# Kernel tuning notes

Hardware: AMD Instinct MI355X
Metric: run time of the kernel (lower is better)

The kernel has to match this reference:

```python
import jax, jax.numpy as jnp
import numpy as np

NNZ = 3355443          # int(4096*4096*(1-0.8))
IN_FEATURES = 4096
OUT_FEATURES = 4096
BATCH = 64
ACTIVE_THRESHOLD = 0.01


def setup_inputs() -> dict:
    key = jax.random.key(0)
    k1, k2, k3, k4 = jax.random.split(key, 4)
    x = jax.random.uniform(k1, (BATCH, IN_FEATURES), dtype=jnp.float32)
    row_indices = jax.random.randint(k2, (NNZ,), 0, OUT_FEATURES, dtype=jnp.int32)
    col_indices = jax.random.randint(k3, (NNZ,), 0, IN_FEATURES, dtype=jnp.int32)
    values = jax.random.normal(k4, (NNZ,), dtype=jnp.float32)
    bias = jnp.zeros((OUT_FEATURES,), dtype=jnp.float32)
    return {"x": x, "row_indices": row_indices, "col_indices": col_indices,
            "values": values, "bias": bias}


def reference(x, row_indices, col_indices, values, bias):
    # Event-driven gating: only columns with x > threshold contribute.
    # Equivalent to masking x, then a standard COO spmv per batch row.
    xm = jnp.where(x > ACTIVE_THRESHOLD, x, jnp.zeros((), x.dtype))   # [B, in]
    contrib = values[None, :] * xm[:, col_indices]                    # [B, nnz]
    out = jnp.zeros((x.shape[0], bias.shape[0]), dtype=x.dtype)
    out = out.at[:, row_indices].add(contrib)                         # scatter-add over rows
    return out + bias[None, :]
```

## Files before the change

### kernel.cpp

```cpp
#include <hip/hip_runtime.h>
#include <hip/hip_bf16.h>
#include <stdint.h>

#define IN_F 4096
#define OUT_F 4096
#define NBKT 256
#define SBLOCKS 410
#define REC_PER_SB 8192
#define SMAX 14336u
#define THRESH 0.01f

typedef unsigned int u32;
typedef unsigned short u16;
typedef unsigned char u8;
typedef __attribute__((ext_vector_type(8))) short short8;
typedef __attribute__((ext_vector_type(4))) float f32x4;

static constexpr size_t pad256(size_t x) { return (x + 255u) & ~(size_t)255u; }
static constexpr size_t WS_XB   = 0;
static constexpr size_t WS_CUR  = pad256(WS_XB + (size_t)512 * 64 * 8 * 2);
static constexpr size_t WS_BINS = pad256(WS_CUR + (size_t)NBKT * 4);
static constexpr size_t WS_NEEDED = WS_BINS + (size_t)NBKT * SMAX * 4;

static __device__ __forceinline__ u16 f2bf(float v) {
  __hip_bfloat16 h = __float2bfloat16(v);
  return *reinterpret_cast<u16*>(&h);
}

__global__ __launch_bounds__(256) void k_init(u32* __restrict__ gcursor) {
  gcursor[threadIdx.x] = 0u;
}

__global__ __launch_bounds__(1024) void k_scatter(const int* __restrict__ rows,
                                                  const int* __restrict__ cols,
                                                  const float* __restrict__ vals, u32 nnz,
                                                  const float* __restrict__ x,
                                                  u16* __restrict__ xB,
                                                  u32* __restrict__ gcursor,
                                                  u32* __restrict__ sortb) {
  __shared__ u32 cnt[NBKT];
  __shared__ u32 pref[NBKT + 1];
  __shared__ u32 gbase[NBKT];
  __shared__ u32 srt[REC_PER_SB];
  __shared__ u8 srtb[REC_PER_SB];
  const int tid = threadIdx.x;
  const int lane = tid & 63;
  const int wid = tid >> 6;

  if (blockIdx.x < 32) {
    const int g = blockIdx.x * 1024 + tid;
    const int b = g & 63;
    const int kg = g >> 6;
    const float* src = x + (size_t)b * IN_F + kg * 8;
    const f32x4 a0 = *reinterpret_cast<const f32x4*>(src);
    const f32x4 a1 = *reinterpret_cast<const f32x4*>(src + 4);
    short8 o;
#pragma unroll
    for (int e = 0; e < 4; ++e) {
      float v = a0[e]; v = (v > THRESH) ? v : 0.0f; o[e] = (short)f2bf(v);
    }
#pragma unroll
    for (int e = 0; e < 4; ++e) {
      float v = a1[e]; v = (v > THRESH) ? v : 0.0f; o[4 + e] = (short)f2bf(v);
    }
    *reinterpret_cast<short8*>(xB + ((size_t)kg * 64 + b) * 8) = o;
  }

  if (tid < NBKT) cnt[tid] = 0;
  __syncthreads();
  const u32 base_i = blockIdx.x * (u32)REC_PER_SB;
  u32 rec[8], bkt[8], rk[8];
#pragma unroll
  for (int j = 0; j < 8; ++j) {
    const u32 i = base_i + (u32)j * 1024u + tid;
    bkt[j] = 0xffffffffu;
    if (i < nnz) {
      const u32 r = (u32)rows[i] & 4095u;
      const u32 c = (u32)cols[i] & 4095u;
      rec[j] = (c << 20) | ((r & 15u) << 16) | (u32)f2bf(vals[i]);
      bkt[j] = r >> 4;
      rk[j] = atomicAdd(&cnt[bkt[j]], 1u);
    }
  }
  __syncthreads();
  if (wid == 0) {
    u32 a[4]; u32 s = 0;
#pragma unroll
    for (int j = 0; j < 4; ++j) { a[j] = cnt[lane * 4 + j]; s += a[j]; }
    u32 xx = s;
#pragma unroll
    for (int d = 1; d < 64; d <<= 1) {
      const u32 y = (u32)__shfl_up((int)xx, d, 64);
      if (lane >= d) xx += y;
    }
    u32 e = xx - s;
#pragma unroll
    for (int j = 0; j < 4; ++j) { pref[lane * 4 + j] = e; e += a[j]; }
    if (lane == 63) pref[256] = e;
  }
  __syncthreads();
#pragma unroll
  for (int j = 0; j < 8; ++j)
    if (bkt[j] != 0xffffffffu) {
      const u32 pos = pref[bkt[j]] + rk[j];
      srt[pos] = rec[j];
      srtb[pos] = (u8)bkt[j];
    }
  if (tid < NBKT) {
    const u32 len = pref[tid + 1] - pref[tid];
    gbase[tid] = len ? atomicAdd(&gcursor[tid], len) : 0u;
  }
  __syncthreads();
  const u32 tot = pref[NBKT];
#pragma unroll
  for (int j = 0; j < 8; ++j) {
    const u32 i = (u32)j * 1024u + tid;
    if (i < tot) {
      const u32 t = srtb[i];
      const u32 off = gbase[t] + (i - pref[t]);
      if (off < SMAX) sortb[(size_t)t * SMAX + off] = srt[i];
    }
  }
}

__global__ __launch_bounds__(1024, 1) void k_accum(const u32* __restrict__ sortb,
                                                   const u32* __restrict__ ntot,
                                                   const u16* __restrict__ xB,
                                                   const float* __restrict__ bias,
                                                   float* __restrict__ out) {
  __shared__ float W[16 * 1024];
  const int tid = threadIdx.x;
  const int lane = tid & 63;
  const int w = tid >> 6;
  const u32 t = blockIdx.x;
  u32 n = ntot[t];
  if (n > SMAX) n = SMAX;
  const u32* bin = sortb + (size_t)t * SMAX;
  u32 rec[14];
#pragma unroll
  for (int j = 0; j < 14; ++j) {
    const u32 i = (u32)j * 1024u + tid;
    rec[j] = (i < n) ? bin[i] : 0u;
  }

  f32x4 acc0 = {0.f, 0.f, 0.f, 0.f}, acc1 = {0.f, 0.f, 0.f, 0.f};
  f32x4 acc2 = {0.f, 0.f, 0.f, 0.f}, acc3 = {0.f, 0.f, 0.f, 0.f};
  const int row = lane & 15;
  const int e8 = (lane >> 4) * 8;

  for (int q = 0; q < 4; ++q) {
    __syncthreads();
    const f32x4 z = {0.f, 0.f, 0.f, 0.f};
#pragma unroll
    for (int j = 0; j < 4; ++j)
      *reinterpret_cast<f32x4*>(&W[j * 4096 + tid * 4]) = z;
    __syncthreads();
#pragma unroll
    for (int j = 0; j < 14; ++j) {
      const u32 i = (u32)j * 1024u + tid;
      if (i < n) {
        const u32 rc = rec[j];
        if ((rc >> 30) == (u32)q) {
          const u32 rl = (rc >> 16) & 15u;
          const u32 cl = ((rc >> 20) & 1023u) ^ ((rl & 7u) << 3);
          __hip_atomic_fetch_add(&W[rl * 1024u + cl], __uint_as_float(rc << 16),
                                 __ATOMIC_RELAXED, __HIP_MEMORY_SCOPE_WORKGROUP);
        }
      }
    }
    __syncthreads();
#pragma unroll
    for (int s = 0; s < 2; ++s) {
      const int klb = w * 64 + s * 32 + e8;
      const int sw = klb ^ ((row & 7) << 3);
      const f32x4 wa = *reinterpret_cast<const f32x4*>(&W[row * 1024 + sw]);
      const f32x4 wb = *reinterpret_cast<const f32x4*>(&W[row * 1024 + (sw + 4)]);
      short8 af;
#pragma unroll
      for (int e = 0; e < 4; ++e) af[e] = (short)f2bf(wa[e]);
#pragma unroll
      for (int e = 0; e < 4; ++e) af[4 + e] = (short)f2bf(wb[e]);
      const int kabs = q * 1024 + klb;
      const u16* bp = xB + (size_t)(kabs >> 3) * 512 + (u32)row * 8;
      const short8 b0 = *reinterpret_cast<const short8*>(bp);
      const short8 b1 = *reinterpret_cast<const short8*>(bp + 128);
      const short8 b2 = *reinterpret_cast<const short8*>(bp + 256);
      const short8 b3 = *reinterpret_cast<const short8*>(bp + 384);
      acc0 = __builtin_amdgcn_mfma_f32_16x16x32_bf16(af, b0, acc0, 0, 0, 0);
      acc1 = __builtin_amdgcn_mfma_f32_16x16x32_bf16(af, b1, acc1, 0, 0, 0);
      acc2 = __builtin_amdgcn_mfma_f32_16x16x32_bf16(af, b2, acc2, 0, 0, 0);
      acc3 = __builtin_amdgcn_mfma_f32_16x16x32_bf16(af, b3, acc3, 0, 0, 0);
    }
  }
  __syncthreads();
  {
    const int ccol = lane & 15;
    const int rb = (lane >> 4) * 4;
#pragma unroll
    for (int qq = 0; qq < 4; ++qq) W[((w * 4 + 0) * 16 + rb + qq) * 16 + ccol] = acc0[qq];
#pragma unroll
    for (int qq = 0; qq < 4; ++qq) W[((w * 4 + 1) * 16 + rb + qq) * 16 + ccol] = acc1[qq];
#pragma unroll
    for (int qq = 0; qq < 4; ++qq) W[((w * 4 + 2) * 16 + rb + qq) * 16 + ccol] = acc2[qq];
#pragma unroll
    for (int qq = 0; qq < 4; ++qq) W[((w * 4 + 3) * 16 + rb + qq) * 16 + ccol] = acc3[qq];
  }
  __syncthreads();
  const int rl = tid & 15;
  const int b = tid >> 4;
  float sum = bias[t * 16u + rl];
#pragma unroll
  for (int w2 = 0; w2 < 16; ++w2)
    sum += W[((w2 * 4 + (b >> 4)) * 16 + rl) * 16 + (b & 15)];
  out[(size_t)b * OUT_F + t * 16u + rl] = sum;
}

__global__ __launch_bounds__(256) void k_bias_init(const float* __restrict__ bias,
                                                   float* __restrict__ out) {
  const int i = blockIdx.x * 256 + threadIdx.x;
  if (i < 64 * OUT_F) out[i] = bias[i & (OUT_F - 1)];
}

__global__ __launch_bounds__(256) void k_fallback(const int* __restrict__ rows,
                                                  const int* __restrict__ cols,
                                                  const float* __restrict__ vals,
                                                  const float* __restrict__ x,
                                                  float* __restrict__ out, int nnz) {
  const int gw = (int)(((u32)blockIdx.x * blockDim.x + threadIdx.x) >> 6);
  const int lane = threadIdx.x & 63;
  const int nw = (int)(((u32)gridDim.x * blockDim.x) >> 6);
  for (int i = gw; i < nnz; i += nw) {
    const int r = rows[i];
    const int c = cols[i];
    const float v = vals[i];
    const float xv = x[lane * IN_F + c];
    if (xv > THRESH) atomicAdd(&out[(size_t)lane * OUT_F + r], v * xv);
  }
}

extern "C" void kernel_launch(void* const* d_in, const int* in_sizes, int n_in,
                              void* d_out, int out_size, void* d_ws, size_t ws_size,
                              hipStream_t stream) {
  const float* x = (const float*)d_in[0];
  const int* rows = (const int*)d_in[1];
  const int* cols = (const int*)d_in[2];
  const float* vals = (const float*)d_in[3];
  const float* bias = (const float*)d_in[4];
  float* out = (float*)d_out;
  const int nnz = in_sizes[1];

  if (ws_size >= WS_NEEDED && nnz <= SBLOCKS * REC_PER_SB) {
    u16* xB = (u16*)((char*)d_ws + WS_XB);
    u32* gcursor = (u32*)((char*)d_ws + WS_CUR);
    u32* sortb = (u32*)((char*)d_ws + WS_BINS);
    k_init<<<1, 256, 0, stream>>>(gcursor);
    k_scatter<<<SBLOCKS, 1024, 0, stream>>>(rows, cols, vals, (u32)nnz, x, xB,
                                            gcursor, sortb);
    k_accum<<<NBKT, 1024, 0, stream>>>(sortb, gcursor, xB, bias, out);
  } else {
    k_bias_init<<<(64 * OUT_F + 255) / 256, 256, 0, stream>>>(bias, out);
    k_fallback<<<4096, 256, 0, stream>>>(rows, cols, vals, x, out, nnz);
  }
}
```

Baseline: 57.11 us.

## Split output rows into 512 buckets of 8 rows for more accumulate blocks

After: 62.89 us. +10.1%, slower.

```diff
diff --git a/kernel.cpp b/kernel.cpp
--- a/kernel.cpp
+++ b/kernel.cpp
@@ -4,15 +4,14 @@
 
 #define IN_F 4096
 #define OUT_F 4096
-#define NBKT 256
+#define NBKT 512
 #define SBLOCKS 410
 #define REC_PER_SB 8192
-#define SMAX 14336u
+#define SMAX 7168u
 #define THRESH 0.01f
 
 typedef unsigned int u32;
 typedef unsigned short u16;
-typedef unsigned char u8;
 typedef __attribute__((ext_vector_type(8))) short short8;
 typedef __attribute__((ext_vector_type(4))) float f32x4;
 
@@ -27,7 +26,7 @@
   return *reinterpret_cast<u16*>(&h);
 }
 
-__global__ __launch_bounds__(256) void k_init(u32* __restrict__ gcursor) {
+__global__ __launch_bounds__(512) void k_init(u32* __restrict__ gcursor) {
   gcursor[threadIdx.x] = 0u;
 }
 
@@ -42,7 +41,7 @@
   __shared__ u32 pref[NBKT + 1];
   __shared__ u32 gbase[NBKT];
   __shared__ u32 srt[REC_PER_SB];
-  __shared__ u8 srtb[REC_PER_SB];
+  __shared__ u16 srtb[REC_PER_SB];
   const int tid = threadIdx.x;
   const int lane = tid & 63;
   const int wid = tid >> 6;
@@ -77,16 +76,16 @@
     if (i < nnz) {
       const u32 r = (u32)rows[i] & 4095u;
       const u32 c = (u32)cols[i] & 4095u;
-      rec[j] = (c << 20) | ((r & 15u) << 16) | (u32)f2bf(vals[i]);
-      bkt[j] = r >> 4;
+      rec[j] = (c << 20) | ((r & 7u) << 16) | (u32)f2bf(vals[i]);
+      bkt[j] = r >> 3;
       rk[j] = atomicAdd(&cnt[bkt[j]], 1u);
     }
   }
   __syncthreads();
   if (wid == 0) {
-    u32 a[4]; u32 s = 0;
-#pragma unroll
-    for (int j = 0; j < 4; ++j) { a[j] = cnt[lane * 4 + j]; s += a[j]; }
+    u32 a[8]; u32 s = 0;
+#pragma unroll
+    for (int j = 0; j < 8; ++j) { a[j] = cnt[lane * 8 + j]; s += a[j]; }
     u32 xx = s;
 #pragma unroll
     for (int d = 1; d < 64; d <<= 1) {
@@ -95,8 +94,8 @@
     }
     u32 e = xx - s;
 #pragma unroll
-    for (int j = 0; j < 4; ++j) { pref[lane * 4 + j] = e; e += a[j]; }
-    if (lane == 63) pref[256] = e;
+    for (int j = 0; j < 8; ++j) { pref[lane * 8 + j] = e; e += a[j]; }
+    if (lane == 63) pref[NBKT] = e;
   }
   __syncthreads();
 #pragma unroll
@@ -104,7 +103,7 @@
     if (bkt[j] != 0xffffffffu) {
       const u32 pos = pref[bkt[j]] + rk[j];
       srt[pos] = rec[j];
-      srtb[pos] = (u8)bkt[j];
+      srtb[pos] = (u16)bkt[j];
     }
   if (tid < NBKT) {
     const u32 len = pref[tid + 1] - pref[tid];
@@ -123,12 +122,12 @@
   }
 }
 
-__global__ __launch_bounds__(1024, 1) void k_accum(const u32* __restrict__ sortb,
+__global__ __launch_bounds__(1024, 8) void k_accum(const u32* __restrict__ sortb,
                                                    const u32* __restrict__ ntot,
                                                    const u16* __restrict__ xB,
                                                    const float* __restrict__ bias,
                                                    float* __restrict__ out) {
-  __shared__ float W[16 * 1024];
+  __shared__ float W[8 * 1024];
   const int tid = threadIdx.x;
   const int lane = tid & 63;
   const int w = tid >> 6;
@@ -136,35 +135,35 @@
   u32 n = ntot[t];
   if (n > SMAX) n = SMAX;
   const u32* bin = sortb + (size_t)t * SMAX;
-  u32 rec[14];
-#pragma unroll
-  for (int j = 0; j < 14; ++j) {
+  u32 rec[7];
+#pragma unroll
+  for (int j = 0; j < 7; ++j) {
     const u32 i = (u32)j * 1024u + tid;
     rec[j] = (i < n) ? bin[i] : 0u;
   }
 
-  f32x4 acc0 = {0.f, 0.f, 0.f, 0.f}, acc1 = {0.f, 0.f, 0.f, 0.f};
-  f32x4 acc2 = {0.f, 0.f, 0.f, 0.f}, acc3 = {0.f, 0.f, 0.f, 0.f};
+  const f32x4 zv = {0.f, 0.f, 0.f, 0.f};
+  f32x4 acc0 = zv, acc1 = zv, acc2 = zv, acc3 = zv;
   const int row = lane & 15;
+  const bool alive = row < 8;
+  const int rw = row & 7;
   const int e8 = (lane >> 4) * 8;
 
   for (int q = 0; q < 4; ++q) {
     __syncthreads();
-    const f32x4 z = {0.f, 0.f, 0.f, 0.f};
-#pragma unroll
-    for (int j = 0; j < 4; ++j)
-      *reinterpret_cast<f32x4*>(&W[j * 4096 + tid * 4]) = z;
+#pragma unroll
+    for (int j = 0; j < 2; ++j)
+      *reinterpret_cast<f32x4*>(&W[j * 4096 + tid * 4]) = zv;
     __syncthreads();
 #pragma unroll
-    for (int j = 0; j < 14; ++j) {
+    for (int j = 0; j < 7; ++j) {
       const u32 i = (u32)j * 1024u + tid;
       if (i < n) {
         const u32 rc = rec[j];
         if ((rc >> 30) == (u32)q) {
-          const u32 rl = (rc >> 16) & 15u;
-          const u32 cl = ((rc >> 20) & 1023u) ^ ((rl & 7u) << 3);
-          __hip_atomic_fetch_add(&W[rl * 1024u + cl], __uint_as_float(rc << 16),
-                                 __ATOMIC_RELAXED, __HIP_MEMORY_SCOPE_WORKGROUP);
+          const u32 rl = (rc >> 16) & 7u;
+          const u32 cl = ((rc >> 20) & 1023u) ^ (rl << 3);
+          unsafeAtomicAdd(&W[rl * 1024u + cl], __uint_as_float(rc << 16));
         }
       }
     }
@@ -172,9 +171,10 @@
 #pragma unroll
     for (int s = 0; s < 2; ++s) {
       const int klb = w * 64 + s * 32 + e8;
-      const int sw = klb ^ ((row & 7) << 3);
-      const f32x4 wa = *reinterpret_cast<const f32x4*>(&W[row * 1024 + sw]);
-      const f32x4 wb = *reinterpret_cast<const f32x4*>(&W[row * 1024 + (sw + 4)]);
+      const int sw = klb ^ (rw << 3);
+      f32x4 wa = *reinterpret_cast<const f32x4*>(&W[rw * 1024 + sw]);
+      f32x4 wb = *reinterpret_cast<const f32x4*>(&W[rw * 1024 + (sw + 4)]);
+      if (!alive) { wa = zv; wb = zv; }
       short8 af;
 #pragma unroll
       for (int e = 0; e < 4; ++e) af[e] = (short)f2bf(wa[e]);
@@ -196,23 +196,27 @@
   {
     const int ccol = lane & 15;
     const int rb = (lane >> 4) * 4;
-#pragma unroll
-    for (int qq = 0; qq < 4; ++qq) W[((w * 4 + 0) * 16 + rb + qq) * 16 + ccol] = acc0[qq];
-#pragma unroll
-    for (int qq = 0; qq < 4; ++qq) W[((w * 4 + 1) * 16 + rb + qq) * 16 + ccol] = acc1[qq];
-#pragma unroll
-    for (int qq = 0; qq < 4; ++qq) W[((w * 4 + 2) * 16 + rb + qq) * 16 + ccol] = acc2[qq];
-#pragma unroll
-    for (int qq = 0; qq < 4; ++qq) W[((w * 4 + 3) * 16 + rb + qq) * 16 + ccol] = acc3[qq];
-  }
-  __syncthreads();
-  const int rl = tid & 15;
-  const int b = tid >> 4;
-  float sum = bias[t * 16u + rl];
-#pragma unroll
-  for (int w2 = 0; w2 < 16; ++w2)
-    sum += W[((w2 * 4 + (b >> 4)) * 16 + rl) * 16 + (b & 15)];
-  out[(size_t)b * OUT_F + t * 16u + rl] = sum;
+    if (rb < 8) {
+#pragma unroll
+      for (int qq = 0; qq < 4; ++qq) W[((w * 4 + 0) * 8 + rb + qq) * 16 + ccol] = acc0[qq];
+#pragma unroll
+      for (int qq = 0; qq < 4; ++qq) W[((w * 4 + 1) * 8 + rb + qq) * 16 + ccol] = acc1[qq];
+#pragma unroll
+      for (int qq = 0; qq < 4; ++qq) W[((w * 4 + 2) * 8 + rb + qq) * 16 + ccol] = acc2[qq];
+#pragma unroll
+      for (int qq = 0; qq < 4; ++qq) W[((w * 4 + 3) * 8 + rb + qq) * 16 + ccol] = acc3[qq];
+    }
+  }
+  __syncthreads();
+  if (tid < 512) {
+    const int rl = tid & 7;
+    const int b = tid >> 3;
+    float sum = bias[t * 8u + rl];
+#pragma unroll
+    for (int w2 = 0; w2 < 16; ++w2)
+      sum += W[((w2 * 4 + (b >> 4)) * 8 + rl) * 16 + (b & 15)];
+    out[(size_t)b * OUT_F + t * 8u + rl] = sum;
+  }
 }
 
 __global__ __launch_bounds__(256) void k_bias_init(const float* __restrict__ bias,
@@ -253,7 +257,7 @@
     u16* xB = (u16*)((char*)d_ws + WS_XB);
     u32* gcursor = (u32*)((char*)d_ws + WS_CUR);
     u32* sortb = (u32*)((char*)d_ws + WS_BINS);
-    k_init<<<1, 256, 0, stream>>>(gcursor);
+    k_init<<<1, 512, 0, stream>>>(gcursor);
     k_scatter<<<SBLOCKS, 1024, 0, stream>>>(rows, cols, vals, (u32)nnz, x, xB,
                                             gcursor, sortb);
     k_accum<<<NBKT, 1024, 0, stream>>>(sortb, gcursor, xB, bias, out);
```

## Split accumulation across two blocks per bucket with atomic output merge

Applied to the files above, without the earlier changes.

New measurement: 59.91 us. 1.05x slower.

```diff
diff --git a/kernel.cpp b/kernel.cpp
--- a/kernel.cpp
+++ b/kernel.cpp
@@ -5,8 +5,8 @@
 #define IN_F 4096
 #define OUT_F 4096
 #define NBKT 256
-#define SBLOCKS 410
-#define REC_PER_SB 8192
+#define SBLOCKS 256
+#define REC_PER_SB 13120
 #define SMAX 14336u
 #define THRESH 0.01f
 
@@ -27,8 +27,12 @@
   return *reinterpret_cast<u16*>(&h);
 }
 
-__global__ __launch_bounds__(256) void k_init(u32* __restrict__ gcursor) {
-  gcursor[threadIdx.x] = 0u;
+__global__ __launch_bounds__(1024) void k_init(u32* __restrict__ gcursor,
+                                               const float* __restrict__ bias,
+                                               float* __restrict__ out) {
+  const int i = blockIdx.x * 1024 + threadIdx.x;
+  out[i] = bias[i & (OUT_F - 1)];
+  if (blockIdx.x == 0 && threadIdx.x < NBKT) gcursor[threadIdx.x] = 0u;
 }
 
 __global__ __launch_bounds__(1024) void k_scatter(const int* __restrict__ rows,
@@ -69,12 +73,13 @@
   if (tid < NBKT) cnt[tid] = 0;
   __syncthreads();
   const u32 base_i = blockIdx.x * (u32)REC_PER_SB;
-  u32 rec[8], bkt[8], rk[8];
-#pragma unroll
-  for (int j = 0; j < 8; ++j) {
-    const u32 i = base_i + (u32)j * 1024u + tid;
+  u32 rec[13], bkt[13], rk[13];
+#pragma unroll
+  for (int j = 0; j < 13; ++j) {
+    const u32 il = (u32)j * 1024u + tid;
+    const u32 i = base_i + il;
     bkt[j] = 0xffffffffu;
-    if (i < nnz) {
+    if (il < (u32)REC_PER_SB && i < nnz) {
       const u32 r = (u32)rows[i] & 4095u;
       const u32 c = (u32)cols[i] & 4095u;
       rec[j] = (c << 20) | ((r & 15u) << 16) | (u32)f2bf(vals[i]);
@@ -96,11 +101,11 @@
     u32 e = xx - s;
 #pragma unroll
     for (int j = 0; j < 4; ++j) { pref[lane * 4 + j] = e; e += a[j]; }
-    if (lane == 63) pref[256] = e;
-  }
-  __syncthreads();
-#pragma unroll
-  for (int j = 0; j < 8; ++j)
+    if (lane == 63) pref[NBKT] = e;
+  }
+  __syncthreads();
+#pragma unroll
+  for (int j = 0; j < 13; ++j)
     if (bkt[j] != 0xffffffffu) {
       const u32 pos = pref[bkt[j]] + rk[j];
       srt[pos] = rec[j];
@@ -113,7 +118,7 @@
   __syncthreads();
   const u32 tot = pref[NBKT];
 #pragma unroll
-  for (int j = 0; j < 8; ++j) {
+  for (int j = 0; j < 13; ++j) {
     const u32 i = (u32)j * 1024u + tid;
     if (i < tot) {
       const u32 t = srtb[i];
@@ -123,16 +128,16 @@
   }
 }
 
-__global__ __launch_bounds__(1024, 1) void k_accum(const u32* __restrict__ sortb,
-                                                   const u32* __restrict__ ntot,
-                                                   const u16* __restrict__ xB,
-                                                   const float* __restrict__ bias,
-                                                   float* __restrict__ out) {
+__global__ __launch_bounds__(1024) void k_accum(const u32* __restrict__ sortb,
+                                                const u32* __restrict__ ntot,
+                                                const u16* __restrict__ xB,
+                                                float* __restrict__ out) {
   __shared__ float W[16 * 1024];
   const int tid = threadIdx.x;
   const int lane = tid & 63;
   const int w = tid >> 6;
-  const u32 t = blockIdx.x;
+  const u32 t = blockIdx.x >> 1;
+  const int h = blockIdx.x & 1;
   u32 n = ntot[t];
   if (n > SMAX) n = SMAX;
   const u32* bin = sortb + (size_t)t * SMAX;
@@ -143,28 +148,27 @@
     rec[j] = (i < n) ? bin[i] : 0u;
   }
 
-  f32x4 acc0 = {0.f, 0.f, 0.f, 0.f}, acc1 = {0.f, 0.f, 0.f, 0.f};
-  f32x4 acc2 = {0.f, 0.f, 0.f, 0.f}, acc3 = {0.f, 0.f, 0.f, 0.f};
+  const f32x4 zv = {0.f, 0.f, 0.f, 0.f};
+  f32x4 acc0 = zv, acc1 = zv, acc2 = zv, acc3 = zv;
   const int row = lane & 15;
   const int e8 = (lane >> 4) * 8;
 
-  for (int q = 0; q < 4; ++q) {
+  for (int qq = 0; qq < 2; ++qq) {
+    const u32 q = (u32)(2 * h + qq);
     __syncthreads();
-    const f32x4 z = {0.f, 0.f, 0.f, 0.f};
 #pragma unroll
     for (int j = 0; j < 4; ++j)
-      *reinterpret_cast<f32x4*>(&W[j * 4096 + tid * 4]) = z;
+      *reinterpret_cast<f32x4*>(&W[j * 4096 + tid * 4]) = zv;
     __syncthreads();
 #pragma unroll
     for (int j = 0; j < 14; ++j) {
       const u32 i = (u32)j * 1024u + tid;
       if (i < n) {
         const u32 rc = rec[j];
-        if ((rc >> 30) == (u32)q) {
+        if ((rc >> 30) == q) {
           const u32 rl = (rc >> 16) & 15u;
           const u32 cl = ((rc >> 20) & 1023u) ^ ((rl & 7u) << 3);
-          __hip_atomic_fetch_add(&W[rl * 1024u + cl], __uint_as_float(rc << 16),
-                                 __ATOMIC_RELAXED, __HIP_MEMORY_SCOPE_WORKGROUP);
+          unsafeAtomicAdd(&W[rl * 1024u + cl], __uint_as_float(rc << 16));
         }
       }
     }
@@ -180,7 +184,7 @@
       for (int e = 0; e < 4; ++e) af[e] = (short)f2bf(wa[e]);
 #pragma unroll
       for (int e = 0; e < 4; ++e) af[4 + e] = (short)f2bf(wb[e]);
-      const int kabs = q * 1024 + klb;
+      const int kabs = (int)q * 1024 + klb;
       const u16* bp = xB + (size_t)(kabs >> 3) * 512 + (u32)row * 8;
       const short8 b0 = *reinterpret_cast<const short8*>(bp);
       const short8 b1 = *reinterpret_cast<const short8*>(bp + 128);
@@ -208,11 +212,11 @@
   __syncthreads();
   const int rl = tid & 15;
   const int b = tid >> 4;
-  float sum = bias[t * 16u + rl];
+  float sum = 0.f;
 #pragma unroll
   for (int w2 = 0; w2 < 16; ++w2)
     sum += W[((w2 * 4 + (b >> 4)) * 16 + rl) * 16 + (b & 15)];
-  out[(size_t)b * OUT_F + t * 16u + rl] = sum;
+  unsafeAtomicAdd(&out[(size_t)b * OUT_F + t * 16u + rl], sum);
 }
 
 __global__ __launch_bounds__(256) void k_bias_init(const float* __restrict__ bias,
@@ -253,10 +257,10 @@
     u16* xB = (u16*)((char*)d_ws + WS_XB);
     u32* gcursor = (u32*)((char*)d_ws + WS_CUR);
     u32* sortb = (u32*)((char*)d_ws + WS_BINS);
-    k_init<<<1, 256, 0, stream>>>(gcursor);
+    k_init<<<256, 1024, 0, stream>>>(gcursor, bias, out);
     k_scatter<<<SBLOCKS, 1024, 0, stream>>>(rows, cols, vals, (u32)nnz, x, xB,
                                             gcursor, sortb);
-    k_accum<<<NBKT, 1024, 0, stream>>>(sortb, gcursor, xB, bias, out);
+    k_accum<<<NBKT * 2, 1024, 0, stream>>>(sortb, gcursor, xB, out);
   } else {
     k_bias_init<<<(64 * OUT_F + 255) / 256, 256, 0, stream>>>(bias, out);
     k_fallback<<<4096, 256, 0, stream>>>(rows, cols, vals, x, out, nnz);
```
